# Optimization experiments

Hardware: AMD Instinct MI355X
Metric: run time of the kernel (lower is better)

## Reference

```python
import jax, jax.numpy as jnp
import numpy as np

NUM_HEADS = 16
DIM_PER_HEAD = 64
DIM = 1024
B, L = 2, 2048
SCALE = DIM_PER_HEAD ** -0.5


def setup_inputs() -> dict:
    key = jax.random.key(0)
    k1, k2, k3, k4, k5 = jax.random.split(key, 5)
    inner = NUM_HEADS * DIM_PER_HEAD
    x = jax.random.normal(k1, (B, L, DIM), dtype=jnp.float32)
    mask = jax.random.randint(k2, (B, L, L), 0, 2, dtype=jnp.int32)
    W_qkv = jax.random.normal(k3, (DIM, 3 * inner), dtype=jnp.float32) * (DIM ** -0.5)
    W_out = jax.random.normal(k4, (inner, DIM), dtype=jnp.float32) * (inner ** -0.5)
    b_out = jax.random.normal(k5, (DIM,), dtype=jnp.float32) * 0.01
    return {"x": x, "mask": mask, "W_qkv": W_qkv, "W_out": W_out, "b_out": b_out}


def reference(x, mask, W_qkv, W_out, b_out):
    b, l, _ = x.shape
    h, d = NUM_HEADS, DIM_PER_HEAD
    # qkv: [b, l, 3, h, d] -> q/k/v each [b, h, l, d]
    qkv = (x @ W_qkv).reshape(b, l, 3, h, d)
    qkv = jnp.transpose(qkv, (2, 0, 3, 1, 4))
    q, k, v = qkv[0], qkv[1], qkv[2]
    scores = jnp.einsum('bhid,bhjd->bhij', q, k) * SCALE
    attn = jax.nn.softmax(scores, axis=-1)
    # post-softmax mask multiply + renormalize (matches original)
    m = mask[:, None, :, :].astype(attn.dtype)
    attn = attn * m
    attn = attn / (attn.sum(axis=-1, keepdims=True) + 1e-10)
    z = jnp.einsum('bhij,bhjd->bhid', attn, v)
    z = jnp.transpose(z, (0, 2, 1, 3)).reshape(b, l, h * d)
    return z @ W_out + b_out
```

## Files before the change

### kernel.cpp

```cpp
#include <hip/hip_runtime.h>

typedef __attribute__((ext_vector_type(8))) short bf16x8;
typedef __attribute__((ext_vector_type(4))) float f32x4;
typedef __attribute__((ext_vector_type(4))) unsigned short us4;
typedef __attribute__((ext_vector_type(4))) unsigned int u32x4;
typedef unsigned short us;

#define C2 0.18033688011112042f

__device__ __forceinline__ unsigned short f2bf(float f) {
    unsigned int u = __float_as_uint(f);
    u = (u + 0x7FFF + ((u >> 16) & 1)) >> 16;
    return (unsigned short)u;
}


__global__ __launch_bounds__(256) void convx(const float* __restrict__ X,
                                             unsigned short* __restrict__ O) {
    int i = blockIdx.x * 256 + threadIdx.x;
    float4 v = ((const float4*)X)[i];
    us4 o;
    o.x = f2bf(v.x); o.y = f2bf(v.y); o.z = f2bf(v.z); o.w = f2bf(v.w);
    ((us4*)O)[i] = o;
}

__global__ __launch_bounds__(256) void transposew(const float* __restrict__ W,
                                                  unsigned short* __restrict__ WT,
                                                  int Kd, int Cd) {
    __shared__ float t[32][33];
    int c0 = blockIdx.x * 32, k0 = blockIdx.y * 32;
    int tx = threadIdx.x & 31, ty = threadIdx.x >> 5;
#pragma unroll
    for (int i = 0; i < 32; i += 8)
        t[ty + i][tx] = W[(size_t)(k0 + ty + i) * Cd + c0 + tx];
    __syncthreads();
#pragma unroll
    for (int i = 0; i < 32; i += 8)
        WT[(size_t)(c0 + ty + i) * Kd + k0 + tx] = f2bf(t[tx][ty + i]);
}

__global__ __launch_bounds__(256) void packmask(const int* __restrict__ Mi,
                                                unsigned int* __restrict__ Mo) {
    int i = blockIdx.x * 256 + threadIdx.x;
    int4 v = ((const int4*)Mi)[i];
    Mo[i] = (unsigned)(v.x & 1) | ((unsigned)(v.y & 1) << 8) |
            ((unsigned)(v.z & 1) << 16) | ((unsigned)(v.w & 1) << 24);
}

template <int MODE>
__global__ __launch_bounds__(256) void gemm_bf16(
    const unsigned short* __restrict__ A, const unsigned short* __restrict__ BT,
    int M, int N, int K,
    unsigned short* __restrict__ Qo, unsigned short* __restrict__ Ko,
    unsigned short* __restrict__ Vo,
    const float* __restrict__ bias, float* __restrict__ Co) {
    __shared__ unsigned short Asub[128 * 64];
    __shared__ unsigned short Bsub[128 * 64];
    const int bm = blockIdx.y, bn = blockIdx.x;
    const int tid = threadIdx.x, w = tid >> 6, lane = tid & 63;
    const int wr = w >> 1, wc = w & 1, l16 = lane & 15, lg = lane >> 4;

    f32x4 acc[4][4];
#pragma unroll
    for (int i = 0; i < 4; i++)
#pragma unroll
        for (int j = 0; j < 4; j++) acc[i][j] = (f32x4){0.f, 0.f, 0.f, 0.f};

    const int wbase = (tid & ~63) * 16;

    const int nkt = K / 64;
    for (int kt = 0; kt < nkt; kt++) {
        const int k0 = kt * 64;
#pragma unroll
        for (int i = 0; i < 4; i++) {
            int slot = i * 256 + tid;
            int r = slot >> 3, blk = slot & 7;
            const us* srcA = A + (size_t)(bm * 128 + r) * K + k0 + ((blk ^ (r & 7)) << 3);
            __builtin_amdgcn_global_load_lds(
                (const __attribute__((address_space(1))) unsigned*)srcA,
                (__attribute__((address_space(3))) unsigned*)((char*)Asub + i * 4096 + wbase),
                16, 0, 0);
            const us* srcB = BT + (size_t)(bn * 128 + r) * K + k0 + ((blk ^ (r & 7)) << 3);
            __builtin_amdgcn_global_load_lds(
                (const __attribute__((address_space(1))) unsigned*)srcB,
                (__attribute__((address_space(3))) unsigned*)((char*)Bsub + i * 4096 + wbase),
                16, 0, 0);
        }
        asm volatile("s_waitcnt vmcnt(0)" ::: "memory");
        __builtin_amdgcn_sched_barrier(0);
        __syncthreads();
#pragma unroll
        for (int ks = 0; ks < 2; ks++) {
            bf16x8 af[4], bfr[4];
            int kk = ks * 32 + lg * 8;
#pragma unroll
            for (int i = 0; i < 4; i++) {
                int r = wr * 64 + i * 16 + l16;
                af[i] = *(bf16x8*)((char*)Asub + ((r * 128 + kk * 2) ^ ((r & 7) << 4)));
                int c = wc * 64 + i * 16 + l16;
                bfr[i] = *(bf16x8*)((char*)Bsub + ((c * 128 + kk * 2) ^ ((c & 7) << 4)));
            }
#pragma unroll
            for (int i = 0; i < 4; i++)
#pragma unroll
                for (int j = 0; j < 4; j++)
                    acc[i][j] = __builtin_amdgcn_mfma_f32_16x16x32_bf16(
                        af[i], bfr[j], acc[i][j], 0, 0, 0);
        }
        __syncthreads();
    }

    if (MODE == 0) {
#pragma unroll
        for (int i = 0; i < 4; i++) {
            int grow = bm * 128 + wr * 64 + i * 16 + lg * 4;
            int bb = grow >> 11, ll = grow & 2047;
#pragma unroll
            for (int j = 0; j < 4; j++) {
                int gcol = bn * 128 + wc * 64 + j * 16 + l16;
                int s = gcol >> 10, hh = (gcol >> 6) & 15, dd = gcol & 63;
                int bhh = bb * 16 + hh;
                if (s == 2) {
                    us4 pk;
                    pk.x = f2bf(acc[i][j][0]); pk.y = f2bf(acc[i][j][1]);
                    pk.z = f2bf(acc[i][j][2]); pk.w = f2bf(acc[i][j][3]);
                    *(us4*)(Vo + (size_t)(bhh * 64 + dd) * 2048 + ll) = pk;
                } else if (s == 0) {
                    unsigned short* dst = Qo + (size_t)(bhh * 2048 + ll) * 64 + dd;
#pragma unroll
                    for (int r = 0; r < 4; r++)
                        dst[(size_t)r * 64] = f2bf(acc[i][j][r] * C2);
                } else {
                    unsigned short* dst = Ko + (size_t)(bhh * 2048 + ll) * 64 + dd;
#pragma unroll
                    for (int r = 0; r < 4; r++) dst[(size_t)r * 64] = f2bf(acc[i][j][r]);
                }
            }
        }
    } else {
#pragma unroll
        for (int i = 0; i < 4; i++) {
            int grow = bm * 128 + wr * 64 + i * 16 + lg * 4;
#pragma unroll
            for (int j = 0; j < 4; j++) {
                int gcol = bn * 128 + wc * 64 + j * 16 + l16;
                float bv = bias[gcol];
#pragma unroll
                for (int r = 0; r < 4; r++)
                    Co[(size_t)(grow + r) * N + gcol] = acc[i][j][r] + bv;
            }
        }
    }
}

__global__ __launch_bounds__(256, 4) void flash_attn(
    const us* __restrict__ Q, const us* __restrict__ Kt,
    const us* __restrict__ VT, const unsigned char* __restrict__ M8,
    us* __restrict__ Z) {
    __shared__ char lds[2][20480];
    const int bh = blockIdx.y;
    const int b = bh >> 4, h = bh & 15;
    const int tid = threadIdx.x, w = tid >> 6, lane = tid & 63;
    const int l16 = lane & 15, lg = lane >> 4;
    const int qb0 = blockIdx.x * 64;
    const int qrow = qb0 + w * 16 + l16;

    const size_t kbh = (size_t)bh * 2048;
    const size_t vbh = (size_t)bh * 64;

    const us* Qp = Q + (size_t)(kbh + qrow) * 64 + lg * 8;
    bf16x8 qf0 = *(const bf16x8*)(Qp);
    bf16x8 qf1 = *(const bf16x8*)(Qp + 32);

    float m_r = -__builtin_inff();
    float l_r = 0.f;
    f32x4 oacc[4];
#pragma unroll
    for (int jd = 0; jd < 4; jd++) oacc[jd] = (f32x4){0.f, 0.f, 0.f, 0.f};

    const int L0 = l16 + (((2 * lg) & 3) << 4);
    const int L1 = l16 + (((2 * lg + 1) & 3) << 4);
    const bool hi = (lg >> 1) != 0;

    int koff[8], voff[8], moff[4];
#pragma unroll
    for (int j = 0; j < 4; j++)
#pragma unroll
        for (int hh = 0; hh < 2; hh++)
            koff[2 * j + hh] = (16 * j + l16) * 128 + ((64 * hh + 16 * lg) ^ ((l16 & 7) << 4));
#pragma unroll
    for (int ks = 0; ks < 2; ks++)
#pragma unroll
        for (int jd = 0; jd < 4; jd++)
            voff[ks * 4 + jd] =
                8192 + (jd * 16 + l16) * 128 + ((64 * ks + 16 * lg) ^ ((l16 & 7) << 4));
#pragma unroll
    for (int j = 0; j < 4; j++)
        moff[j] = 16384 + (w * 16 + l16) * 64 + ((16 * j + 4 * lg) ^ ((l16 & 3) << 4));

    const int wbase = (tid & ~63) * 16;

    auto STAGE = [&](int bufi, int kt) {
        char* base = &lds[bufi][0];
        const int lk = kt * 64;
#pragma unroll
        for (int i = 0; i < 2; i++) {
            int slot = i * 256 + tid;
            int r = slot >> 3, blk = slot & 7;
            const us* src = Kt + (kbh + lk + r) * 64 + ((blk ^ (r & 7)) << 3);
            __builtin_amdgcn_global_load_lds(
                (const __attribute__((address_space(1))) unsigned*)src,
                (__attribute__((address_space(3))) unsigned*)(base + i * 4096 + wbase),
                16, 0, 0);
        }
#pragma unroll
        for (int i = 0; i < 2; i++) {
            int slot = i * 256 + tid;
            int r = slot >> 3, blk = slot & 7;
            const us* src = VT + (vbh + r) * 2048 + lk + ((blk ^ (r & 7)) << 3);
            __builtin_amdgcn_global_load_lds(
                (const __attribute__((address_space(1))) unsigned*)src,
                (__attribute__((address_space(3))) unsigned*)(base + 8192 + i * 4096 + wbase),
                16, 0, 0);
        }
        {
            int r = tid >> 2, mb = tid & 3;
            const unsigned char* src =
                M8 + (size_t)(b * 2048 + qb0 + r) * 2048 + lk + ((mb ^ (r & 3)) << 4);
            __builtin_amdgcn_global_load_lds(
                (const __attribute__((address_space(1))) unsigned*)src,
                (__attribute__((address_space(3))) unsigned*)(base + 16384 + wbase),
                16, 0, 0);
        }
    };

    STAGE(0, 0);
    asm volatile("s_waitcnt vmcnt(0) lgkmcnt(0)" ::: "memory");
    __builtin_amdgcn_sched_barrier(0);
    __syncthreads();
    int cur = 0;

    for (int kt = 0; kt < 32; kt++) {
        if (kt < 31) STAGE(cur ^ 1, kt + 1);
        char* Lb = &lds[cur][0];
        unsigned mw[4];
#pragma unroll
        for (int j = 0; j < 4; j++) mw[j] = *(const unsigned*)(Lb + moff[j]);
        bf16x8 kf[8];
#pragma unroll
        for (int q8 = 0; q8 < 8; q8++) kf[q8] = *(const bf16x8*)(Lb + koff[q8]);
        f32x4 sacc[4];
#pragma unroll
        for (int j = 0; j < 4; j++) sacc[j] = (f32x4){0.f, 0.f, 0.f, 0.f};
#pragma unroll
        for (int j = 0; j < 4; j++) {
            sacc[j] = __builtin_amdgcn_mfma_f32_16x16x32_bf16(kf[2 * j], qf0, sacc[j], 0, 0, 0);
            sacc[j] = __builtin_amdgcn_mfma_f32_16x16x32_bf16(kf[2 * j + 1], qf1, sacc[j], 0, 0, 0);
        }
        float mx0 = fmaxf(fmaxf(sacc[0][0], sacc[0][1]), fmaxf(sacc[0][2], sacc[0][3]));
        float mx1 = fmaxf(fmaxf(sacc[1][0], sacc[1][1]), fmaxf(sacc[1][2], sacc[1][3]));
        float mx2 = fmaxf(fmaxf(sacc[2][0], sacc[2][1]), fmaxf(sacc[2][2], sacc[2][3]));
        float mx3 = fmaxf(fmaxf(sacc[3][0], sacc[3][1]), fmaxf(sacc[3][2], sacc[3][3]));
        float mx = fmaxf(fmaxf(mx0, mx1), fmaxf(mx2, mx3));
        mx = fmaxf(mx, __shfl_xor(mx, 16));
        mx = fmaxf(mx, __shfl_xor(mx, 32));
        if (mx > m_r + 8.f) {
            float alpha = __builtin_amdgcn_exp2f(m_r - mx);
            m_r = mx;
            l_r *= alpha;
#pragma unroll
            for (int jd = 0; jd < 4; jd++) {
                oacc[jd][0] *= alpha; oacc[jd][1] *= alpha;
                oacc[jd][2] *= alpha; oacc[jd][3] *= alpha;
            }
        }
        unsigned W[4][2];
        float rs = 0.f;
#pragma unroll
        for (int j = 0; j < 4; j++) {
            uchar4 mu = __builtin_bit_cast(uchar4, mw[j]);
            float p0 = __builtin_amdgcn_exp2f(sacc[j][0] - m_r) * (float)mu.x;
            float p1 = __builtin_amdgcn_exp2f(sacc[j][1] - m_r) * (float)mu.y;
            float p2 = __builtin_amdgcn_exp2f(sacc[j][2] - m_r) * (float)mu.z;
            float p3 = __builtin_amdgcn_exp2f(sacc[j][3] - m_r) * (float)mu.w;
            rs += (p0 + p1) + (p2 + p3);
            W[j][0] = __builtin_amdgcn_perm(__float_as_uint(p1), __float_as_uint(p0),
                                            0x07060302u);
            W[j][1] = __builtin_amdgcn_perm(__float_as_uint(p3), __float_as_uint(p2),
                                            0x07060302u);
        }
        rs += __shfl_xor(rs, 16);
        rs += __shfl_xor(rs, 32);
        l_r += rs;
#pragma unroll
        for (int ks = 0; ks < 2; ks++) {
            bf16x8 vf[4];
#pragma unroll
            for (int jd = 0; jd < 4; jd++)
                vf[jd] = *(const bf16x8*)(Lb + voff[ks * 4 + jd]);
            unsigned a0 = __shfl((int)W[2 * ks][0], L0), b0 = __shfl((int)W[2 * ks + 1][0], L0);
            unsigned a1 = __shfl((int)W[2 * ks][1], L0), b1 = __shfl((int)W[2 * ks + 1][1], L0);
            unsigned a2 = __shfl((int)W[2 * ks][0], L1), b2 = __shfl((int)W[2 * ks + 1][0], L1);
            unsigned a3 = __shfl((int)W[2 * ks][1], L1), b3 = __shfl((int)W[2 * ks + 1][1], L1);
            u32x4 pw = (u32x4){hi ? b0 : a0, hi ? b1 : a1, hi ? b2 : a2, hi ? b3 : a3};
            bf16x8 pB = __builtin_bit_cast(bf16x8, pw);
#pragma unroll
            for (int jd = 0; jd < 4; jd++)
                oacc[jd] = __builtin_amdgcn_mfma_f32_16x16x32_bf16(vf[jd], pB,
                                                                   oacc[jd], 0, 0, 0);
        }
        asm volatile("s_waitcnt vmcnt(0) lgkmcnt(0)" ::: "memory");
        __builtin_amdgcn_sched_barrier(0);
        __syncthreads();
        cur ^= 1;
    }

    const float inv = 1.0f / (l_r + 1e-20f);
    us* zp = Z + (size_t)(b * 2048 + qrow) * 1024 + h * 64 + lg * 4;
#pragma unroll
    for (int jd = 0; jd < 4; jd++) {
        us4 pk;
        pk.x = f2bf(oacc[jd][0] * inv);
        pk.y = f2bf(oacc[jd][1] * inv);
        pk.z = f2bf(oacc[jd][2] * inv);
        pk.w = f2bf(oacc[jd][3] * inv);
        *(us4*)(zp + jd * 16) = pk;
    }
}


extern "C" void kernel_launch(void* const* d_in, const int* in_sizes, int n_in,
                              void* d_out, int out_size, void* d_ws, size_t ws_size,
                              hipStream_t stream) {
    const float* x = (const float*)d_in[0];
    const int* mask = (const int*)d_in[1];
    const float* Wqkv = (const float*)d_in[2];
    const float* Wout = (const float*)d_in[3];
    const float* bout = (const float*)d_in[4];
    float* out = (float*)d_out;
    char* ws = (char*)d_ws;

    unsigned short* xz    = (unsigned short*)(ws);
    unsigned short* wqkvT = (unsigned short*)(ws + (8u << 20));
    unsigned short* woutT = (unsigned short*)(ws + (14u << 20));
    unsigned char*  m8    = (unsigned char*)(ws + (16u << 20));
    unsigned short* Qb    = (unsigned short*)(ws + (24u << 20));
    unsigned short* Kb    = (unsigned short*)(ws + (32u << 20));
    unsigned short* VTb   = (unsigned short*)(ws + (40u << 20));

    convx<<<4096, 256, 0, stream>>>(x, xz);
    transposew<<<dim3(3072 / 32, 1024 / 32), 256, 0, stream>>>(Wqkv, wqkvT, 1024, 3072);
    transposew<<<dim3(1024 / 32, 1024 / 32), 256, 0, stream>>>(Wout, woutT, 1024, 1024);
    packmask<<<8192, 256, 0, stream>>>(mask, (unsigned int*)m8);
    gemm_bf16<0><<<dim3(3072 / 128, 4096 / 128), 256, 0, stream>>>(
        xz, wqkvT, 4096, 3072, 1024, Qb, Kb, VTb, nullptr, nullptr);
    flash_attn<<<dim3(32, 32), 256, 0, stream>>>(Qb, Kb, VTb, m8, xz);
    gemm_bf16<1><<<dim3(1024 / 128, 4096 / 128), 256, 0, stream>>>(
        xz, woutT, 4096, 1024, 1024, nullptr, nullptr, nullptr, bout, out);
}
```

Before: 175.8 us.

## Register-prefetch next GEMM k-tile to overlap global loads with MFMA

```diff
diff --git a/kernel.cpp b/kernel.cpp
--- a/kernel.cpp
+++ b/kernel.cpp
@@ -66,29 +66,37 @@
 #pragma unroll
         for (int j = 0; j < 4; j++) acc[i][j] = (f32x4){0.f, 0.f, 0.f, 0.f};
 
-    const int wbase = (tid & ~63) * 16;
-
+    const int r_st = tid >> 3;
+    const int kc_st = (tid & 7) * 8;
     const int nkt = K / 64;
+
+    uint4 va[4], vb[4];
+#pragma unroll
+    for (int i = 0; i < 4; i++) {
+        int r = r_st + i * 32;
+        va[i] = *(const uint4*)(A + (size_t)(bm * 128 + r) * K + kc_st);
+        vb[i] = *(const uint4*)(BT + (size_t)(bn * 128 + r) * K + kc_st);
+    }
+
     for (int kt = 0; kt < nkt; kt++) {
-        const int k0 = kt * 64;
 #pragma unroll
         for (int i = 0; i < 4; i++) {
-            int slot = i * 256 + tid;
-            int r = slot >> 3, blk = slot & 7;
-            const us* srcA = A + (size_t)(bm * 128 + r) * K + k0 + ((blk ^ (r & 7)) << 3);
-            __builtin_amdgcn_global_load_lds(
-                (const __attribute__((address_space(1))) unsigned*)srcA,
-                (__attribute__((address_space(3))) unsigned*)((char*)Asub + i * 4096 + wbase),
-                16, 0, 0);
-            const us* srcB = BT + (size_t)(bn * 128 + r) * K + k0 + ((blk ^ (r & 7)) << 3);
-            __builtin_amdgcn_global_load_lds(
-                (const __attribute__((address_space(1))) unsigned*)srcB,
-                (__attribute__((address_space(3))) unsigned*)((char*)Bsub + i * 4096 + wbase),
-                16, 0, 0);
-        }
-        asm volatile("s_waitcnt vmcnt(0)" ::: "memory");
+            int r = r_st + i * 32;
+            int byt = (r * 128 + kc_st * 2) ^ ((r & 7) << 4);
+            *(uint4*)((char*)Asub + byt) = va[i];
+            *(uint4*)((char*)Bsub + byt) = vb[i];
+        }
+        __syncthreads();
+        if (kt < nkt - 1) {
+            const int k0 = (kt + 1) * 64;
+#pragma unroll
+            for (int i = 0; i < 4; i++) {
+                int r = r_st + i * 32;
+                va[i] = *(const uint4*)(A + (size_t)(bm * 128 + r) * K + k0 + kc_st);
+                vb[i] = *(const uint4*)(BT + (size_t)(bn * 128 + r) * K + k0 + kc_st);
+            }
+        }
         __builtin_amdgcn_sched_barrier(0);
-        __syncthreads();
 #pragma unroll
         for (int ks = 0; ks < 2; ks++) {
             bf16x8 af[4], bfr[4];
```

Measured after the change: 262.9 us. 49.5% more time.
